# Performance work log

Hardware: AMD Instinct MI355X
Metric: run time of the kernel (lower is better)

Reference implementation:

```python
import jax, jax.numpy as jnp
import numpy as np

ALPHA = 1.702  # sigmoid slope in clamped-GLU
LIMIT = 7.0    # clamp limit on gate/up

B, S, H, D, E, K = 2, 2048, 1024, 1024, 8, 2


def setup_inputs() -> dict:
    key = jax.random.key(0)
    ks = jax.random.split(key, 7)
    hidden_states = jax.random.normal(ks[0], (B, S, H), jnp.float32)
    router_indices = jax.random.randint(ks[1], (B * S, K), 0, E)
    routing_weights = jax.random.uniform(ks[2], (B * S, E), dtype=jnp.float32)
    gate_up_proj = jax.random.normal(ks[3], (E, H, 2 * D), jnp.float32) * 0.02
    gate_up_bias = jax.random.normal(ks[4], (E, 2 * D), jnp.float32) * 0.02
    down_proj = jax.random.normal(ks[5], (E, D, H), jnp.float32) * 0.02
    down_bias = jax.random.normal(ks[6], (E, H), jnp.float32) * 0.02
    return dict(hidden_states=hidden_states, router_indices=router_indices,
                routing_weights=routing_weights, gate_up_proj=gate_up_proj,
                gate_up_bias=gate_up_bias, down_proj=down_proj, down_bias=down_bias)


def reference(hidden_states, router_indices, routing_weights,
              gate_up_proj, gate_up_bias, down_proj, down_bias):
    batch = hidden_states.shape[0]
    hs = hidden_states.shape[-1]
    flat = hidden_states.reshape(-1, hs)  # [T, H]
    n_exp = routing_weights.shape[1]
    # index_add with possibly duplicated (token, expert) assignments == count multiplier
    counts = (router_indices[:, :, None] == jnp.arange(n_exp)[None, None, :]).sum(1)  # [T, E]
    w = routing_weights * counts.astype(flat.dtype)  # [T, E] effective combine weight

    def step(out, xs):
        wgu, bgu, wd, bd, we = xs  # wgu:[H,2D] bgu:[2D] wd:[D,H] bd:[H] we:[T]
        gu = flat @ wgu + bgu                      # [T, 2D]
        gate = jnp.minimum(gu[:, ::2], LIMIT)      # interleaved gate channels
        up = jnp.clip(gu[:, 1::2], -LIMIT, LIMIT)  # interleaved up channels
        mid = (up + 1.0) * gate * jax.nn.sigmoid(gate * ALPHA)
        y = mid @ wd + bd                          # [T, H]
        return out + y * we[:, None], None

    out0 = jnp.zeros_like(flat)
    out, _ = jax.lax.scan(step, out0, (gate_up_proj, gate_up_bias, down_proj, down_bias, w.T))
    return out.reshape(batch, -1, hs)
```

## Files before the change

kernel.cpp:

```cpp
#include <hip/hip_runtime.h>
#include <hip/hip_bf16.h>

#define AS1 __attribute__((address_space(1)))
#define AS3 __attribute__((address_space(3)))

typedef __bf16 bf16_8 __attribute__((ext_vector_type(8)));
typedef float f32x4 __attribute__((ext_vector_type(4)));

constexpr int Tn = 4096;
constexpr int Hn = 1024;
constexpr int Dn = 1024;
constexpr int En = 8;
constexpr int Pmax = 9216;
constexpr int MaxTiles = 72;
constexpr float kAlpha = 1.702f;
constexpr float kLimit = 7.0f;

__device__ __forceinline__ unsigned short f2bf(float x) {
  unsigned u = __builtin_bit_cast(unsigned, x);
  u = u + 0x7FFFu + ((u >> 16) & 1u);
  return (unsigned short)(u >> 16);
}
__device__ __forceinline__ unsigned pack2(float a, float b) {
  return (unsigned)f2bf(a) | ((unsigned)f2bf(b) << 16);
}
__device__ __forceinline__ float bflo(unsigned v) { return __builtin_bit_cast(float, v << 16); }
__device__ __forceinline__ float bfhi(unsigned v) { return __builtin_bit_cast(float, v & 0xFFFF0000u); }

__device__ __forceinline__ void gload_lds16(const void* gp, void* lp) {
  __builtin_amdgcn_global_load_lds(
      (const AS1 unsigned int*)(unsigned long long)gp,
      (AS3 unsigned int*)(unsigned int)(unsigned long long)lp,
      16, 0, 0);
}

constexpr int NB_CVT = 4096, NB_TGU = 4096, NB_TDN = 4096;

__global__ void k_prepass(const float* __restrict__ hs, const int* __restrict__ ridx,
                          const float* __restrict__ gup, const float* __restrict__ dwn,
                          unsigned short* __restrict__ xb,
                          unsigned short* __restrict__ wg, unsigned short* __restrict__ wu,
                          unsigned short* __restrict__ wdt,
                          int* __restrict__ tix, int* __restrict__ pos,
                          int* __restrict__ tileE, int* __restrict__ tileP0,
                          int* __restrict__ ntiles) {
  __shared__ __align__(16) char smem[2 * 32 * 65 * 4 + 64];
  const int tid = threadIdx.x;
  int b = blockIdx.x;

  if (b == 0) {
    int (*lh)[8] = (int(*)[8])smem;
    int* eoff = (int*)(smem + 8192);
#pragma unroll
    for (int e = 0; e < 8; e++) lh[tid][e] = 0;
    int myE[32];
#pragma unroll
    for (int s = 0; s < 32; s++) {
      int e = ridx[tid * 32 + s];
      myE[s] = e;
      lh[tid][e]++;
    }
    __syncthreads();
    if (tid < 8) {
      int tot = 0;
#pragma unroll 1
      for (int t = 0; t < 256; t++) { int v = lh[t][tid]; lh[t][tid] = tot; tot += v; }
      eoff[tid] = tot;
    }
    __syncthreads();
    if (tid == 0) {
      int off = 0, nt = 0;
#pragma unroll 1
      for (int e = 0; e < 8; e++) {
        int cnt = eoff[e];
        eoff[e] = off;
        int nt128 = (cnt + 127) >> 7;
        for (int k = 0; k < nt128; k++) { tileE[nt] = e; tileP0[nt] = off + k * 128; nt++; }
        off += nt128 * 128;
      }
      *ntiles = nt;
    }
    __syncthreads();
    for (int p = tid; p < Pmax; p += 256) tix[p] = 0;
    __syncthreads();
#pragma unroll
    for (int s = 0; s < 32; s++) {
      int slot = tid * 32 + s;
      int e = myE[s];
      int p = eoff[e] + (lh[tid][e]++);
      pos[slot] = p;
      tix[p] = slot >> 1;
    }
    return;
  }
  b -= 1;

  if (b < NB_CVT) {
    int i = b * 256 + tid;
    float4 v = reinterpret_cast<const float4*>(hs)[i];
    ushort4 o;
    o.x = f2bf(v.x); o.y = f2bf(v.y); o.z = f2bf(v.z); o.w = f2bf(v.w);
    reinterpret_cast<ushort4*>(xb)[i] = o;
    return;
  }
  b -= NB_CVT;

  if (b < NB_TGU) {
    float (*lg)[65] = (float(*)[65])smem;
    float (*lu)[65] = (float(*)[65])(smem + 32 * 65 * 4);
    const int d0 = (b & 31) * 32, h0 = ((b >> 5) & 15) * 64, e = b >> 9;
    {
      const int hrow = tid >> 2, q = tid & 3;
      const float* src = gup + ((size_t)e * Hn + h0 + hrow) * (2 * Dn) + d0 * 2 + q * 16;
#pragma unroll
      for (int j = 0; j < 4; j++) {
        float4 v = *reinterpret_cast<const float4*>(src + j * 4);
        int dp = q * 8 + j * 2;
        lg[dp][hrow] = v.x; lu[dp][hrow] = v.y;
        lg[dp + 1][hrow] = v.z; lu[dp + 1][hrow] = v.w;
      }
    }
    __syncthreads();
    {
      const int d = tid >> 3, hc = (tid & 7) * 8;
      uint4 og, ou;
      og.x = pack2(lg[d][hc + 0], lg[d][hc + 1]); ou.x = pack2(lu[d][hc + 0], lu[d][hc + 1]);
      og.y = pack2(lg[d][hc + 2], lg[d][hc + 3]); ou.y = pack2(lu[d][hc + 2], lu[d][hc + 3]);
      og.z = pack2(lg[d][hc + 4], lg[d][hc + 5]); ou.z = pack2(lu[d][hc + 4], lu[d][hc + 5]);
      og.w = pack2(lg[d][hc + 6], lg[d][hc + 7]); ou.w = pack2(lu[d][hc + 6], lu[d][hc + 7]);
      *reinterpret_cast<uint4*>(wg + ((size_t)e * Dn + d0 + d) * Hn + h0 + hc) = og;
      *reinterpret_cast<uint4*>(wu + ((size_t)e * Dn + d0 + d) * Hn + h0 + hc) = ou;
    }
    return;
  }
  b -= NB_TGU;

  {
    float (*lt)[65] = (float(*)[65])smem;
    const int h0 = (b & 31) * 32, d0 = ((b >> 5) & 15) * 64, e = b >> 9;
    {
      const int drow = tid >> 2, q = tid & 3;
      const float* src = dwn + ((size_t)e * Dn + d0 + drow) * Hn + h0 + q * 8;
#pragma unroll
      for (int j = 0; j < 2; j++) {
        float4 v = *reinterpret_cast<const float4*>(src + j * 4);
        int hr = q * 8 + j * 4;
        lt[hr][drow] = v.x; lt[hr + 1][drow] = v.y; lt[hr + 2][drow] = v.z; lt[hr + 3][drow] = v.w;
      }
    }
    __syncthreads();
    {
      const int h = tid >> 3, dc = (tid & 7) * 8;
      uint4 o;
      o.x = pack2(lt[h][dc + 0], lt[h][dc + 1]);
      o.y = pack2(lt[h][dc + 2], lt[h][dc + 3]);
      o.z = pack2(lt[h][dc + 4], lt[h][dc + 5]);
      o.w = pack2(lt[h][dc + 6], lt[h][dc + 7]);
      *reinterpret_cast<uint4*>(wdt + ((size_t)e * Hn + h0 + h) * Dn + d0 + dc) = o;
    }
  }
}

__launch_bounds__(256, 2)
__global__ void k_gemm1(const unsigned short* __restrict__ xb,
                        const unsigned short* __restrict__ wg,
                        const unsigned short* __restrict__ wu,
                        const float* __restrict__ gub,
                        const int* __restrict__ tix,
                        const int* __restrict__ tileE,
                        const int* __restrict__ tileP0,
                        const int* __restrict__ ntiles,
                        unsigned short* __restrict__ midc) {
  constexpr int BM = 128, BN = 64, BK = 64;
  __shared__ __align__(16) unsigned short Xs[BM * BK];
  __shared__ __align__(16) unsigned short Gs[BN * BK];
  __shared__ __align__(16) unsigned short Us[BN * BK];
  const int nwg = gridDim.x * gridDim.y;
  const int orig = blockIdx.y * gridDim.x + blockIdx.x;
  const int wgid = (orig & 7) * (nwg >> 3) + (orig >> 3);
  const int bx = wgid % gridDim.x;
  const int by = wgid / gridDim.x;
  if (bx >= *ntiles) return;
  const int e = tileE[bx];
  const int p0 = tileP0[bx];
  const int n0 = by * BN;
  const int tid = threadIdx.x;
  const int wv = tid >> 6, lane = tid & 63;
  const int wr = wv >> 1, wc = wv & 1;
  const int r8 = lane >> 3, c8 = lane & 7;

  int tokc[4];
#pragma unroll
  for (int c = 0; c < 4; c++) tokc[c] = tix[p0 + (c * 4 + wv) * 8 + r8];

  const unsigned short* Gp = wg + ((size_t)e * Dn + n0) * Hn;
  const unsigned short* Up = wu + ((size_t)e * Dn + n0) * Hn;

  f32x4 ag[4][2], au[4][2];
#pragma unroll
  for (int i = 0; i < 4; i++)
#pragma unroll
    for (int j = 0; j < 2; j++) { ag[i][j] = f32x4{0.f,0.f,0.f,0.f}; au[i][j] = f32x4{0.f,0.f,0.f,0.f}; }

  for (int k0 = 0; k0 < Hn; k0 += BK) {
#pragma unroll
    for (int c = 0; c < 4; c++) {
      int ch = c * 4 + wv;
      gload_lds16(xb + (size_t)tokc[c] * Hn + k0 + c8 * 8, (void*)(Xs + ch * 512));
    }
#pragma unroll
    for (int c = 0; c < 2; c++) {
      int ch = c * 4 + wv;
      gload_lds16(Gp + (size_t)(ch * 8 + r8) * Hn + k0 + c8 * 8, (void*)(Gs + ch * 512));
      gload_lds16(Up + (size_t)(ch * 8 + r8) * Hn + k0 + c8 * 8, (void*)(Us + ch * 512));
    }
    asm volatile("s_waitcnt vmcnt(0)" ::: "memory");
    __syncthreads();
    const int fr = lane & 15, kg = lane >> 4;
#pragma unroll
    for (int kk = 0; kk < 2; kk++) {
      bf16_8 a[4], bg[2], bu[2];
#pragma unroll
      for (int i = 0; i < 4; i++)
        a[i] = *reinterpret_cast<const bf16_8*>(Xs + (wr * 64 + i * 16 + fr) * BK + kk * 32 + kg * 8);
#pragma unroll
      for (int j = 0; j < 2; j++) {
        bg[j] = *reinterpret_cast<const bf16_8*>(Gs + (wc * 32 + j * 16 + fr) * BK + kk * 32 + kg * 8);
        bu[j] = *reinterpret_cast<const bf16_8*>(Us + (wc * 32 + j * 16 + fr) * BK + kk * 32 + kg * 8);
      }
#pragma unroll
      for (int i = 0; i < 4; i++)
#pragma unroll
        for (int j = 0; j < 2; j++) {
          ag[i][j] = __builtin_amdgcn_mfma_f32_16x16x32_bf16(a[i], bg[j], ag[i][j], 0, 0, 0);
          au[i][j] = __builtin_amdgcn_mfma_f32_16x16x32_bf16(a[i], bu[j], au[i][j], 0, 0, 0);
        }
    }
    __syncthreads();
  }

  const int fr = lane & 15, rg = lane >> 4;
#pragma unroll
  for (int i = 0; i < 4; i++) {
#pragma unroll
    for (int r = 0; r < 4; r++) {
      int row = p0 + wr * 64 + i * 16 + rg * 4 + r;
#pragma unroll
      for (int j = 0; j < 2; j++) {
        int d = n0 + wc * 32 + j * 16 + fr;
        float g = ag[i][j][r] + gub[e * 2 * Dn + 2 * d];
        float u = au[i][j][r] + gub[e * 2 * Dn + 2 * d + 1];
        g = fminf(g, kLimit);
        u = fminf(fmaxf(u, -kLimit), kLimit);
        float sg = 1.0f / (1.0f + __expf(-kAlpha * g));
        float mid = (u + 1.0f) * g * sg;
        midc[(size_t)row * Dn + d] = f2bf(mid);
      }
    }
  }
}

__launch_bounds__(256, 2)
__global__ void k_gemm2(const unsigned short* __restrict__ midc,
                        const unsigned short* __restrict__ wdt,
                        const int* __restrict__ tileE,
                        const int* __restrict__ tileP0,
                        const int* __restrict__ ntiles,
                        unsigned short* __restrict__ ys) {
  constexpr int BM = 128, BN = 64, BK = 64;
  __shared__ __align__(16) unsigned short As[BM * BK];
  __shared__ __align__(16) unsigned short Bs[BN * BK];
  const int nwg = gridDim.x * gridDim.y;
  const int orig = blockIdx.y * gridDim.x + blockIdx.x;
  const int wgid = (orig & 7) * (nwg >> 3) + (orig >> 3);
  const int bx = wgid % gridDim.x;
  const int by = wgid / gridDim.x;
  if (bx >= *ntiles) return;
  const int e = tileE[bx];
  const int p0 = tileP0[bx];
  const int n0 = by * BN;
  const int tid = threadIdx.x;
  const int wv = tid >> 6, lane = tid & 63;
  const int wr = wv >> 1, wc = wv & 1;
  const int r8 = lane >> 3, c8 = lane & 7;
  const unsigned short* Ap = midc + (size_t)p0 * Dn;
  const unsigned short* Bp = wdt + ((size_t)e * Hn + n0) * Dn;

  f32x4 acc[4][2];
#pragma unroll
  for (int i = 0; i < 4; i++)
#pragma unroll
    for (int j = 0; j < 2; j++) acc[i][j] = f32x4{0.f,0.f,0.f,0.f};

  for (int k0 = 0; k0 < Dn; k0 += BK) {
#pragma unroll
    for (int c = 0; c < 4; c++) {
      int ch = c * 4 + wv;
      gload_lds16(Ap + (size_t)(ch * 8 + r8) * Dn + k0 + c8 * 8, (void*)(As + ch * 512));
    }
#pragma unroll
    for (int c = 0; c < 2; c++) {
      int ch = c * 4 + wv;
      gload_lds16(Bp + (size_t)(ch * 8 + r8) * Dn + k0 + c8 * 8, (void*)(Bs + ch * 512));
    }
    asm volatile("s_waitcnt vmcnt(0)" ::: "memory");
    __syncthreads();
    const int fr = lane & 15, kg = lane >> 4;
#pragma unroll
    for (int kk = 0; kk < 2; kk++) {
      bf16_8 a[4], b[2];
#pragma unroll
      for (int i = 0; i < 4; i++)
        a[i] = *reinterpret_cast<const bf16_8*>(As + (wr * 64 + i * 16 + fr) * BK + kk * 32 + kg * 8);
#pragma unroll
      for (int j = 0; j < 2; j++)
        b[j] = *reinterpret_cast<const bf16_8*>(Bs + (wc * 32 + j * 16 + fr) * BK + kk * 32 + kg * 8);
#pragma unroll
      for (int i = 0; i < 4; i++)
#pragma unroll
        for (int j = 0; j < 2; j++)
          acc[i][j] = __builtin_amdgcn_mfma_f32_16x16x32_bf16(a[i], b[j], acc[i][j], 0, 0, 0);
    }
    __syncthreads();
  }

  const int fr = lane & 15, rg = lane >> 4;
#pragma unroll
  for (int i = 0; i < 4; i++)
#pragma unroll
    for (int r = 0; r < 4; r++) {
      int row = p0 + wr * 64 + i * 16 + rg * 4 + r;
#pragma unroll
      for (int j = 0; j < 2; j++) {
        int col = n0 + wc * 32 + j * 16 + fr;
        ys[(size_t)row * Hn + col] = f2bf(acc[i][j][r]);
      }
    }
}

__global__ void k_combine(const unsigned short* __restrict__ ys, const int* __restrict__ ridx,
                          const float* __restrict__ rw, const int* __restrict__ pos,
                          const float* __restrict__ db, float* __restrict__ out) {
  int idx = blockIdx.x * blockDim.x + threadIdx.x;
  int t = idx >> 7, hc = (idx & 127) << 3;
  int e0 = ridx[2 * t], e1 = ridx[2 * t + 1];
  int p0 = pos[2 * t], p1 = pos[2 * t + 1];
  float w0 = rw[t * En + e0], w1 = rw[t * En + e1];
  uint4 ya = *reinterpret_cast<const uint4*>(ys + (size_t)p0 * Hn + hc);
  uint4 yb = *reinterpret_cast<const uint4*>(ys + (size_t)p1 * Hn + hc);
  float4 da0 = *reinterpret_cast<const float4*>(db + (size_t)e0 * Hn + hc);
  float4 da1 = *reinterpret_cast<const float4*>(db + (size_t)e0 * Hn + hc + 4);
  float4 db0 = *reinterpret_cast<const float4*>(db + (size_t)e1 * Hn + hc);
  float4 db1 = *reinterpret_cast<const float4*>(db + (size_t)e1 * Hn + hc + 4);
  float4 o0, o1;
  o0.x = w0 * (bflo(ya.x) + da0.x) + w1 * (bflo(yb.x) + db0.x);
  o0.y = w0 * (bfhi(ya.x) + da0.y) + w1 * (bfhi(yb.x) + db0.y);
  o0.z = w0 * (bflo(ya.y) + da0.z) + w1 * (bflo(yb.y) + db0.z);
  o0.w = w0 * (bfhi(ya.y) + da0.w) + w1 * (bfhi(yb.y) + db0.w);
  o1.x = w0 * (bflo(ya.z) + da1.x) + w1 * (bflo(yb.z) + db1.x);
  o1.y = w0 * (bfhi(ya.z) + da1.y) + w1 * (bfhi(yb.z) + db1.y);
  o1.z = w0 * (bflo(ya.w) + da1.z) + w1 * (bflo(yb.w) + db1.z);
  o1.w = w0 * (bfhi(ya.w) + da1.w) + w1 * (bfhi(yb.w) + db1.w);
  *reinterpret_cast<float4*>(out + (size_t)t * Hn + hc) = o0;
  *reinterpret_cast<float4*>(out + (size_t)t * Hn + hc + 4) = o1;
}

extern "C" void kernel_launch(void* const* d_in, const int* in_sizes, int n_in,
                              void* d_out, int out_size, void* d_ws, size_t ws_size,
                              hipStream_t stream) {
  (void)in_sizes; (void)n_in; (void)out_size; (void)ws_size;
  const float* hs  = (const float*)d_in[0];
  const int*   ri  = (const int*)d_in[1];
  const float* rw  = (const float*)d_in[2];
  const float* gup = (const float*)d_in[3];
  const float* gub = (const float*)d_in[4];
  const float* dwn = (const float*)d_in[5];
  const float* db  = (const float*)d_in[6];
  float* out = (float*)d_out;

  char* ws = (char*)d_ws;
  int* tix    = (int*)(ws);
  int* pos    = (int*)(ws + 65536);
  int* tileE  = (int*)(ws + 131072);
  int* tileP0 = (int*)(ws + 131584);
  int* ntiles = (int*)(ws + 132096);
  unsigned short* xb   = (unsigned short*)(ws + 262144);
  unsigned short* wg   = (unsigned short*)(ws + 262144 + 8388608);
  unsigned short* wu   = (unsigned short*)(ws + 262144 + 8388608 + 16777216);
  unsigned short* wdt  = (unsigned short*)(ws + 262144 + 8388608 + 2*16777216);
  unsigned short* midc = (unsigned short*)(ws + 262144 + 8388608 + 3*16777216);
  unsigned short* ys   = (unsigned short*)(ws + 262144 + 8388608 + 3*16777216 + (size_t)Pmax * Dn * 2);

  k_prepass<<<dim3(1 + NB_CVT + NB_TGU + NB_TDN), dim3(256), 0, stream>>>(
      hs, ri, gup, dwn, xb, wg, wu, wdt, tix, pos, tileE, tileP0, ntiles);
  k_gemm1<<<dim3(MaxTiles, Dn / 64), dim3(256), 0, stream>>>(
      xb, wg, wu, gub, tix, tileE, tileP0, ntiles, midc);
  k_gemm2<<<dim3(MaxTiles, Hn / 64), dim3(256), 0, stream>>>(
      midc, wdt, tileE, tileP0, ntiles, ys);
  k_combine<<<dim3(Tn * Hn / 8 / 256), dim3(256), 0, stream>>>(ys, ri, rw, pos, db, out);
}
```

Before: 142.1 us.

## Move down-proj weight transpose into GEMM1 launch to overlap with compute

Takes the down-projection weight transpose/convert blocks out of the prepass kernel and appends them as extra blocks of the first grouped GEMM launch, so the memory-bound conversion can run alongside the MFMA work of GEMM1. GEMM1 now uses a 1D grid with a manual tile swizzle. The gate/up bias loads are also hoisted out of the epilogue loop. Extra blocks in the GEMM launch compete for CU slots and may delay GEMM tiles, and the shared memory buffer is now a union sized for the GEMM.

```diff
diff --git a/kernel.cpp b/kernel.cpp
--- a/kernel.cpp
+++ b/kernel.cpp
@@ -35,12 +35,12 @@
 }
 
 constexpr int NB_CVT = 4096, NB_TGU = 4096, NB_TDN = 4096;
+constexpr int NG1 = MaxTiles * (Dn / 64);
 
 __global__ void k_prepass(const float* __restrict__ hs, const int* __restrict__ ridx,
-                          const float* __restrict__ gup, const float* __restrict__ dwn,
+                          const float* __restrict__ gup,
                           unsigned short* __restrict__ xb,
                           unsigned short* __restrict__ wg, unsigned short* __restrict__ wu,
-                          unsigned short* __restrict__ wdt,
                           int* __restrict__ tix, int* __restrict__ pos,
                           int* __restrict__ tileE, int* __restrict__ tileP0,
                           int* __restrict__ ntiles) {
@@ -105,7 +105,7 @@
   }
   b -= NB_CVT;
 
-  if (b < NB_TGU) {
+  {
     float (*lg)[65] = (float(*)[65])smem;
     float (*lu)[65] = (float(*)[65])(smem + 32 * 65 * 4);
     const int d0 = (b & 31) * 32, h0 = ((b >> 5) & 15) * 64, e = b >> 9;
@@ -131,11 +131,27 @@
       *reinterpret_cast<uint4*>(wg + ((size_t)e * Dn + d0 + d) * Hn + h0 + hc) = og;
       *reinterpret_cast<uint4*>(wu + ((size_t)e * Dn + d0 + d) * Hn + h0 + hc) = ou;
     }
-    return;
-  }
-  b -= NB_TGU;
-
-  {
+  }
+}
+
+__launch_bounds__(256, 2)
+__global__ void k_main1(const unsigned short* __restrict__ xb,
+                        const unsigned short* __restrict__ wg,
+                        const unsigned short* __restrict__ wu,
+                        const float* __restrict__ gub,
+                        const int* __restrict__ tix,
+                        const int* __restrict__ tileE,
+                        const int* __restrict__ tileP0,
+                        const int* __restrict__ ntiles,
+                        unsigned short* __restrict__ midc,
+                        const float* __restrict__ dwn,
+                        unsigned short* __restrict__ wdt) {
+  constexpr int BM = 128, BN = 64, BK = 64;
+  __shared__ __align__(16) char smem[(BM + 2 * BN) * BK * 2];
+  const int tid = threadIdx.x;
+
+  if ((int)blockIdx.x >= NG1) {
+    int b = blockIdx.x - NG1;
     float (*lt)[65] = (float(*)[65])smem;
     const int h0 = (b & 31) * 32, d0 = ((b >> 5) & 15) * 64, e = b >> 9;
     {
@@ -158,33 +174,20 @@
       o.w = pack2(lt[h][dc + 6], lt[h][dc + 7]);
       *reinterpret_cast<uint4*>(wdt + ((size_t)e * Hn + h0 + h) * Dn + d0 + dc) = o;
     }
-  }
-}
-
-__launch_bounds__(256, 2)
-__global__ void k_gemm1(const unsigned short* __restrict__ xb,
-                        const unsigned short* __restrict__ wg,
-                        const unsigned short* __restrict__ wu,
-                        const float* __restrict__ gub,
-                        const int* __restrict__ tix,
-                        const int* __restrict__ tileE,
-                        const int* __restrict__ tileP0,
-                        const int* __restrict__ ntiles,
-                        unsigned short* __restrict__ midc) {
-  constexpr int BM = 128, BN = 64, BK = 64;
-  __shared__ __align__(16) unsigned short Xs[BM * BK];
-  __shared__ __align__(16) unsigned short Gs[BN * BK];
-  __shared__ __align__(16) unsigned short Us[BN * BK];
-  const int nwg = gridDim.x * gridDim.y;
-  const int orig = blockIdx.y * gridDim.x + blockIdx.x;
-  const int wgid = (orig & 7) * (nwg >> 3) + (orig >> 3);
-  const int bx = wgid % gridDim.x;
-  const int by = wgid / gridDim.x;
+    return;
+  }
+
+  unsigned short* Xs = (unsigned short*)smem;
+  unsigned short* Gs = (unsigned short*)(smem + BM * BK * 2);
+  unsigned short* Us = (unsigned short*)(smem + (BM + BN) * BK * 2);
+  const int orig = blockIdx.x;
+  const int wgid = (orig & 7) * (NG1 >> 3) + (orig >> 3);
+  const int bx = wgid % MaxTiles;
+  const int by = wgid / MaxTiles;
   if (bx >= *ntiles) return;
   const int e = tileE[bx];
   const int p0 = tileP0[bx];
   const int n0 = by * BN;
-  const int tid = threadIdx.x;
   const int wv = tid >> 6, lane = tid & 63;
   const int wr = wv >> 1, wc = wv & 1;
   const int r8 = lane >> 3, c8 = lane & 7;
@@ -240,6 +243,10 @@
   }
 
   const int fr = lane & 15, rg = lane >> 4;
+  const float* gb = gub + e * 2 * Dn;
+  const int dA = n0 + wc * 32 + fr, dB = dA + 16;
+  const float gbiasA = gb[2 * dA], ubiasA = gb[2 * dA + 1];
+  const float gbiasB = gb[2 * dB], ubiasB = gb[2 * dB + 1];
 #pragma unroll
   for (int i = 0; i < 4; i++) {
 #pragma unroll
@@ -247,9 +254,9 @@
       int row = p0 + wr * 64 + i * 16 + rg * 4 + r;
 #pragma unroll
       for (int j = 0; j < 2; j++) {
-        int d = n0 + wc * 32 + j * 16 + fr;
-        float g = ag[i][j][r] + gub[e * 2 * Dn + 2 * d];
-        float u = au[i][j][r] + gub[e * 2 * Dn + 2 * d + 1];
+        int d = j ? dB : dA;
+        float g = ag[i][j][r] + (j ? gbiasB : gbiasA);
+        float u = au[i][j][r] + (j ? ubiasB : ubiasA);
         g = fminf(g, kLimit);
         u = fminf(fmaxf(u, -kLimit), kLimit);
         float sg = 1.0f / (1.0f + __expf(-kAlpha * g));
@@ -391,10 +398,10 @@
   unsigned short* midc = (unsigned short*)(ws + 262144 + 8388608 + 3*16777216);
   unsigned short* ys   = (unsigned short*)(ws + 262144 + 8388608 + 3*16777216 + (size_t)Pmax * Dn * 2);
 
-  k_prepass<<<dim3(1 + NB_CVT + NB_TGU + NB_TDN), dim3(256), 0, stream>>>(
-      hs, ri, gup, dwn, xb, wg, wu, wdt, tix, pos, tileE, tileP0, ntiles);
-  k_gemm1<<<dim3(MaxTiles, Dn / 64), dim3(256), 0, stream>>>(
-      xb, wg, wu, gub, tix, tileE, tileP0, ntiles, midc);
+  k_prepass<<<dim3(1 + NB_CVT + NB_TGU), dim3(256), 0, stream>>>(
+      hs, ri, gup, xb, wg, wu, tix, pos, tileE, tileP0, ntiles);
+  k_main1<<<dim3(NG1 + NB_TDN), dim3(256), 0, stream>>>(
+      xb, wg, wu, gub, tix, tileE, tileP0, ntiles, midc, dwn, wdt);
   k_gemm2<<<dim3(MaxTiles, Hn / 64), dim3(256), 0, stream>>>(
       midc, wdt, tileE, tileP0, ntiles, ys);
   k_combine<<<dim3(Tn * Hn / 8 / 256), dim3(256), 0, stream>>>(ys, ri, rw, pos, db, out);
```

Measured after the change: 138.7 us. 2.4% less time.

## Rewrite gate/up GEMM with 256x128 tiles, double-buffered LDS and split-phase pipeline

Applied to the files above, without the earlier changes.

The first grouped GEMM now uses 512-thread blocks computing 256-token by 128-channel tiles. Its LDS buffers are double-buffered, and global-to-LDS loads for the next K step are issued in four phases interleaved with MFMA groups, using partial vmcnt waits and raw barriers. The routing prepass now pads each expert to 256-row tiles and emits a second 128-row tile list so the down-projection GEMM keeps its old tiling. The goal is to hide load latency and raise MFMA reuse per loaded byte, at the cost of more padding rows, much more LDS and fewer resident blocks.

```diff
diff --git a/kernel.cpp b/kernel.cpp
--- a/kernel.cpp
+++ b/kernel.cpp
@@ -11,8 +11,9 @@
 constexpr int Hn = 1024;
 constexpr int Dn = 1024;
 constexpr int En = 8;
-constexpr int Pmax = 9216;
-constexpr int MaxTiles = 72;
+constexpr int Pmax = 10240;
+constexpr int MaxT256 = 40;
+constexpr int MaxT128 = 80;
 constexpr float kAlpha = 1.702f;
 constexpr float kLimit = 7.0f;
 
@@ -43,7 +44,8 @@
                           unsigned short* __restrict__ wdt,
                           int* __restrict__ tix, int* __restrict__ pos,
                           int* __restrict__ tileE, int* __restrict__ tileP0,
-                          int* __restrict__ ntiles) {
+                          int* __restrict__ tileE2, int* __restrict__ tileP02,
+                          int* __restrict__ ntiles, int* __restrict__ ntiles2) {
   __shared__ __align__(16) char smem[2 * 32 * 65 * 4 + 64];
   const int tid = threadIdx.x;
   int b = blockIdx.x;
@@ -69,16 +71,21 @@
     }
     __syncthreads();
     if (tid == 0) {
-      int off = 0, nt = 0;
+      int off = 0, nt = 0, nt2 = 0;
 #pragma unroll 1
       for (int e = 0; e < 8; e++) {
         int cnt = eoff[e];
         eoff[e] = off;
-        int nt128 = (cnt + 127) >> 7;
-        for (int k = 0; k < nt128; k++) { tileE[nt] = e; tileP0[nt] = off + k * 128; nt++; }
-        off += nt128 * 128;
+        int ntT = (cnt + 255) >> 8;
+        for (int k = 0; k < ntT; k++) {
+          tileE[nt] = e; tileP0[nt] = off + k * 256; nt++;
+          tileE2[nt2] = e; tileP02[nt2] = off + k * 256; nt2++;
+          tileE2[nt2] = e; tileP02[nt2] = off + k * 256 + 128; nt2++;
+        }
+        off += ntT * 256;
       }
       *ntiles = nt;
+      *ntiles2 = nt2;
     }
     __syncthreads();
     for (int p = tid; p < Pmax; p += 256) tix[p] = 0;
@@ -161,7 +168,7 @@
   }
 }
 
-__launch_bounds__(256, 2)
+__launch_bounds__(512, 1)
 __global__ void k_gemm1(const unsigned short* __restrict__ xb,
                         const unsigned short* __restrict__ wg,
                         const unsigned short* __restrict__ wu,
@@ -171,85 +178,157 @@
                         const int* __restrict__ tileP0,
                         const int* __restrict__ ntiles,
                         unsigned short* __restrict__ midc) {
-  constexpr int BM = 128, BN = 64, BK = 64;
-  __shared__ __align__(16) unsigned short Xs[BM * BK];
-  __shared__ __align__(16) unsigned short Gs[BN * BK];
-  __shared__ __align__(16) unsigned short Us[BN * BK];
-  const int nwg = gridDim.x * gridDim.y;
-  const int orig = blockIdx.y * gridDim.x + blockIdx.x;
+  __shared__ __align__(16) unsigned short As0[256 * 64], As1[256 * 64];
+  __shared__ __align__(16) unsigned short Gs0[128 * 64], Gs1[128 * 64];
+  __shared__ __align__(16) unsigned short Us0[128 * 64], Us1[128 * 64];
+
+  const int nwg = gridDim.x;
+  const int orig = blockIdx.x;
   const int wgid = (orig & 7) * (nwg >> 3) + (orig >> 3);
-  const int bx = wgid % gridDim.x;
-  const int by = wgid / gridDim.x;
+  const int bx = wgid % MaxT256;
+  const int by = wgid / MaxT256;
   if (bx >= *ntiles) return;
   const int e = tileE[bx];
   const int p0 = tileP0[bx];
-  const int n0 = by * BN;
+  const int n0 = by * 128;
+
   const int tid = threadIdx.x;
   const int wv = tid >> 6, lane = tid & 63;
-  const int wr = wv >> 1, wc = wv & 1;
-  const int r8 = lane >> 3, c8 = lane & 7;
-
-  int tokc[4];
-#pragma unroll
-  for (int c = 0; c < 4; c++) tokc[c] = tix[p0 + (c * 4 + wv) * 8 + r8];
+  const int wr = wv >> 2, wc = wv & 3;
+  const int l8 = lane >> 3, c8 = lane & 7;
+  const int fr = lane & 15, kg = lane >> 4;
+
+  int tokc[2][2];
+#pragma unroll
+  for (int q = 0; q < 2; q++)
+#pragma unroll
+    for (int l = 0; l < 2; l++)
+      tokc[q][l] = tix[p0 + q * 128 + (wv * 2 + l) * 8 + l8];
 
   const unsigned short* Gp = wg + ((size_t)e * Dn + n0) * Hn;
   const unsigned short* Up = wu + ((size_t)e * Dn + n0) * Hn;
 
-  f32x4 ag[4][2], au[4][2];
-#pragma unroll
-  for (int i = 0; i < 4; i++)
+  auto stageA = [&](int q, unsigned short* dst, int k0) {
+#pragma unroll
+    for (int l = 0; l < 2; l++) {
+      int rl = q * 128 + (wv * 2 + l) * 8;
+      gload_lds16(xb + (size_t)tokc[q][l] * Hn + k0 + c8 * 8, (void*)(dst + rl * 64));
+    }
+  };
+  auto stageB = [&](const unsigned short* src, unsigned short* dst, int k0) {
+#pragma unroll
+    for (int l = 0; l < 2; l++) {
+      int rl = (wv * 2 + l) * 8;
+      gload_lds16(src + (size_t)(rl + l8) * Hn + k0 + c8 * 8, (void*)(dst + rl * 64));
+    }
+  };
+
+  f32x4 ag[8][2], au[8][2];
+#pragma unroll
+  for (int i = 0; i < 8; i++)
 #pragma unroll
     for (int j = 0; j < 2; j++) { ag[i][j] = f32x4{0.f,0.f,0.f,0.f}; au[i][j] = f32x4{0.f,0.f,0.f,0.f}; }
 
-  for (int k0 = 0; k0 < Hn; k0 += BK) {
-#pragma unroll
-    for (int c = 0; c < 4; c++) {
-      int ch = c * 4 + wv;
-      gload_lds16(xb + (size_t)tokc[c] * Hn + k0 + c8 * 8, (void*)(Xs + ch * 512));
-    }
-#pragma unroll
-    for (int c = 0; c < 2; c++) {
-      int ch = c * 4 + wv;
-      gload_lds16(Gp + (size_t)(ch * 8 + r8) * Hn + k0 + c8 * 8, (void*)(Gs + ch * 512));
-      gload_lds16(Up + (size_t)(ch * 8 + r8) * Hn + k0 + c8 * 8, (void*)(Us + ch * 512));
-    }
-    asm volatile("s_waitcnt vmcnt(0)" ::: "memory");
-    __syncthreads();
-    const int fr = lane & 15, kg = lane >> 4;
-#pragma unroll
-    for (int kk = 0; kk < 2; kk++) {
-      bf16_8 a[4], bg[2], bu[2];
-#pragma unroll
-      for (int i = 0; i < 4; i++)
-        a[i] = *reinterpret_cast<const bf16_8*>(Xs + (wr * 64 + i * 16 + fr) * BK + kk * 32 + kg * 8);
+  stageA(0, As0, 0);
+  stageA(1, As0, 0);
+  stageB(Gp, Gs0, 0);
+  stageB(Up, Us0, 0);
+
+  constexpr int NSTEP = 16;
+  for (int t = 0; t < NSTEP; ++t) {
+    const int cur = t & 1;
+    unsigned short* Ac = cur ? As1 : As0;
+    unsigned short* Gc = cur ? Gs1 : Gs0;
+    unsigned short* Uc = cur ? Us1 : Us0;
+    unsigned short* An = cur ? As0 : As1;
+    unsigned short* Gn = cur ? Gs0 : Gs1;
+    unsigned short* Un = cur ? Us0 : Us1;
+    const int kn = ((t + 1) & (NSTEP - 1)) * 64;
+
+    bf16_8 aK0[8], aK1[8], bg0[2], bg1[2], bu0[2], bu1[2];
+
+    stageA(0, An, kn);
+    asm volatile("s_waitcnt vmcnt(4)" ::: "memory");
+    __builtin_amdgcn_s_barrier();
+#pragma unroll
+    for (int i = 0; i < 8; i++)
+      aK0[i] = *reinterpret_cast<const bf16_8*>(Ac + (wr * 128 + i * 16 + fr) * 64 + kg * 8);
+#pragma unroll
+    for (int j = 0; j < 2; j++)
+      bg0[j] = *reinterpret_cast<const bf16_8*>(Gc + (wc * 32 + j * 16 + fr) * 64 + kg * 8);
+    __builtin_amdgcn_s_setprio(1);
+#pragma unroll
+    for (int i = 0; i < 8; i++)
+#pragma unroll
+      for (int j = 0; j < 2; j++)
+        ag[i][j] = __builtin_amdgcn_mfma_f32_16x16x32_bf16(aK0[i], bg0[j], ag[i][j], 0, 0, 0);
+    __builtin_amdgcn_s_setprio(0);
+
+    stageA(1, An, kn);
+    asm volatile("s_waitcnt vmcnt(6)" ::: "memory");
+    __builtin_amdgcn_s_barrier();
+#pragma unroll
+    for (int i = 0; i < 8; i++)
+      aK1[i] = *reinterpret_cast<const bf16_8*>(Ac + (wr * 128 + i * 16 + fr) * 64 + 32 + kg * 8);
+#pragma unroll
+    for (int j = 0; j < 2; j++)
+      bg1[j] = *reinterpret_cast<const bf16_8*>(Gc + (wc * 32 + j * 16 + fr) * 64 + 32 + kg * 8);
+    __builtin_amdgcn_s_setprio(1);
+#pragma unroll
+    for (int i = 0; i < 8; i++)
+#pragma unroll
+      for (int j = 0; j < 2; j++)
+        ag[i][j] = __builtin_amdgcn_mfma_f32_16x16x32_bf16(aK1[i], bg1[j], ag[i][j], 0, 0, 0);
+    __builtin_amdgcn_s_setprio(0);
+
+    stageB(Gp, Gn, kn);
+    asm volatile("s_waitcnt vmcnt(6)" ::: "memory");
+    __builtin_amdgcn_s_barrier();
+#pragma unroll
+    for (int j = 0; j < 2; j++)
+      bu0[j] = *reinterpret_cast<const bf16_8*>(Uc + (wc * 32 + j * 16 + fr) * 64 + kg * 8);
+    __builtin_amdgcn_s_setprio(1);
+#pragma unroll
+    for (int i = 0; i < 8; i++)
+#pragma unroll
+      for (int j = 0; j < 2; j++)
+        au[i][j] = __builtin_amdgcn_mfma_f32_16x16x32_bf16(aK0[i], bu0[j], au[i][j], 0, 0, 0);
+    __builtin_amdgcn_s_setprio(0);
+
+    stageB(Up, Un, kn);
+    asm volatile("s_waitcnt vmcnt(8)" ::: "memory");
+    __builtin_amdgcn_s_barrier();
+#pragma unroll
+    for (int j = 0; j < 2; j++)
+      bu1[j] = *reinterpret_cast<const bf16_8*>(Uc + (wc * 32 + j * 16 + fr) * 64 + 32 + kg * 8);
+    __builtin_amdgcn_s_setprio(1);
+#pragma unroll
+    for (int i = 0; i < 8; i++)
+#pragma unroll
+      for (int j = 0; j < 2; j++)
+        au[i][j] = __builtin_amdgcn_mfma_f32_16x16x32_bf16(aK1[i], bu1[j], au[i][j], 0, 0, 0);
+    __builtin_amdgcn_s_setprio(0);
+
+    asm volatile("s_waitcnt lgkmcnt(0)" ::: "memory");
+    __builtin_amdgcn_s_barrier();
+  }
+  asm volatile("s_waitcnt vmcnt(0)" ::: "memory");
+
+  const int rg = kg;
+  const float* gb = gub + e * 2 * Dn;
+  const int dA = n0 + wc * 32 + fr, dB = dA + 16;
+  const float gbiasA = gb[2 * dA], ubiasA = gb[2 * dA + 1];
+  const float gbiasB = gb[2 * dB], ubiasB = gb[2 * dB + 1];
+#pragma unroll
+  for (int i = 0; i < 8; i++) {
+#pragma unroll
+    for (int r = 0; r < 4; r++) {
+      int row = p0 + wr * 128 + i * 16 + rg * 4 + r;
 #pragma unroll
       for (int j = 0; j < 2; j++) {
-        bg[j] = *reinterpret_cast<const bf16_8*>(Gs + (wc * 32 + j * 16 + fr) * BK + kk * 32 + kg * 8);
-        bu[j] = *reinterpret_cast<const bf16_8*>(Us + (wc * 32 + j * 16 + fr) * BK + kk * 32 + kg * 8);
-      }
-#pragma unroll
-      for (int i = 0; i < 4; i++)
-#pragma unroll
-        for (int j = 0; j < 2; j++) {
-          ag[i][j] = __builtin_amdgcn_mfma_f32_16x16x32_bf16(a[i], bg[j], ag[i][j], 0, 0, 0);
-          au[i][j] = __builtin_amdgcn_mfma_f32_16x16x32_bf16(a[i], bu[j], au[i][j], 0, 0, 0);
-        }
-    }
-    __syncthreads();
-  }
-
-  const int fr = lane & 15, rg = lane >> 4;
-#pragma unroll
-  for (int i = 0; i < 4; i++) {
-#pragma unroll
-    for (int r = 0; r < 4; r++) {
-      int row = p0 + wr * 64 + i * 16 + rg * 4 + r;
-#pragma unroll
-      for (int j = 0; j < 2; j++) {
-        int d = n0 + wc * 32 + j * 16 + fr;
-        float g = ag[i][j][r] + gub[e * 2 * Dn + 2 * d];
-        float u = au[i][j][r] + gub[e * 2 * Dn + 2 * d + 1];
+        int d = j ? dB : dA;
+        float g = ag[i][j][r] + (j ? gbiasB : gbiasA);
+        float u = au[i][j][r] + (j ? ubiasB : ubiasA);
         g = fminf(g, kLimit);
         u = fminf(fmaxf(u, -kLimit), kLimit);
         float sg = 1.0f / (1.0f + __expf(-kAlpha * g));
@@ -263,9 +342,9 @@
 __launch_bounds__(256, 2)
 __global__ void k_gemm2(const unsigned short* __restrict__ midc,
                         const unsigned short* __restrict__ wdt,
-                        const int* __restrict__ tileE,
-                        const int* __restrict__ tileP0,
-                        const int* __restrict__ ntiles,
+                        const int* __restrict__ tileE2,
+                        const int* __restrict__ tileP02,
+                        const int* __restrict__ ntiles2,
                         unsigned short* __restrict__ ys) {
   constexpr int BM = 128, BN = 64, BK = 64;
   __shared__ __align__(16) unsigned short As[BM * BK];
@@ -275,9 +354,9 @@
   const int wgid = (orig & 7) * (nwg >> 3) + (orig >> 3);
   const int bx = wgid % gridDim.x;
   const int by = wgid / gridDim.x;
-  if (bx >= *ntiles) return;
-  const int e = tileE[bx];
-  const int p0 = tileP0[bx];
+  if (bx >= *ntiles2) return;
+  const int e = tileE2[bx];
+  const int p0 = tileP02[bx];
   const int n0 = by * BN;
   const int tid = threadIdx.x;
   const int wv = tid >> 6, lane = tid & 63;
@@ -379,11 +458,14 @@
   float* out = (float*)d_out;
 
   char* ws = (char*)d_ws;
-  int* tix    = (int*)(ws);
-  int* pos    = (int*)(ws + 65536);
-  int* tileE  = (int*)(ws + 131072);
-  int* tileP0 = (int*)(ws + 131584);
-  int* ntiles = (int*)(ws + 132096);
+  int* tix     = (int*)(ws);
+  int* pos     = (int*)(ws + 65536);
+  int* tileE   = (int*)(ws + 131072);
+  int* tileP0  = (int*)(ws + 131584);
+  int* tileE2  = (int*)(ws + 132096);
+  int* tileP02 = (int*)(ws + 132608);
+  int* ntiles  = (int*)(ws + 133120);
+  int* ntiles2 = (int*)(ws + 133124);
   unsigned short* xb   = (unsigned short*)(ws + 262144);
   unsigned short* wg   = (unsigned short*)(ws + 262144 + 8388608);
   unsigned short* wu   = (unsigned short*)(ws + 262144 + 8388608 + 16777216);
@@ -392,10 +474,10 @@
   unsigned short* ys   = (unsigned short*)(ws + 262144 + 8388608 + 3*16777216 + (size_t)Pmax * Dn * 2);
 
   k_prepass<<<dim3(1 + NB_CVT + NB_TGU + NB_TDN), dim3(256), 0, stream>>>(
-      hs, ri, gup, dwn, xb, wg, wu, wdt, tix, pos, tileE, tileP0, ntiles);
-  k_gemm1<<<dim3(MaxTiles, Dn / 64), dim3(256), 0, stream>>>(
+      hs, ri, gup, dwn, xb, wg, wu, wdt, tix, pos, tileE, tileP0, tileE2, tileP02, ntiles, ntiles2);
+  k_gemm1<<<dim3(MaxT256 * (Dn / 128)), dim3(512), 0, stream>>>(
       xb, wg, wu, gub, tix, tileE, tileP0, ntiles, midc);
-  k_gemm2<<<dim3(MaxTiles, Hn / 64), dim3(256), 0, stream>>>(
-      midc, wdt, tileE, tileP0, ntiles, ys);
+  k_gemm2<<<dim3(MaxT128, Hn / 64), dim3(256), 0, stream>>>(
+      midc, wdt, tileE2, tileP02, ntiles2, ys);
   k_combine<<<dim3(Tn * Hn / 8 / 256), dim3(256), 0, stream>>>(ys, ri, rw, pos, db, out);
 }
```

Result: slower. 175.2 us (+23.3%).
